# Kernel optimization log

Hardware: AMD Instinct MI355X
Metric: run time of the kernel (lower is better)

## Reference

```python
import jax, jax.numpy as jnp
import numpy as np

C = 4  # n_features_per_level
RES = [128, 256, 512, 1024]  # base_resolution=128, per_level_scale=2, n_levels=4


def grid_sample(grid, pts):
    """Bilinear grid_sample, align_corners=False, zero padding.
    grid: (B, C, H, W); pts: (B, N, 2) with pts[...,0]=x (width), pts[...,1]=y (height).
    Returns (B, C, N)."""
    B, Cc, H, W = grid.shape
    fx = (pts[..., 0] + 1.0) * 0.5 * W - 0.5
    fy = (pts[..., 1] + 1.0) * 0.5 * H - 0.5
    x0 = jnp.floor(fx)
    y0 = jnp.floor(fy)
    wx = (fx - x0)[:, None, :]
    wy = (fy - y0)[:, None, :]
    x0 = x0.astype(jnp.int32)
    y0 = y0.astype(jnp.int32)

    def corner(xi, yi):
        valid = ((xi >= 0) & (xi < W) & (yi >= 0) & (yi < H)).astype(grid.dtype)
        xc = jnp.clip(xi, 0, W - 1)
        yc = jnp.clip(yi, 0, H - 1)
        vals = jax.vmap(lambda g, yy, xx: g[:, yy, xx])(grid, yc, xc)  # (B, C, N)
        return vals * valid[:, None, :]

    v00 = corner(x0, y0)
    v10 = corner(x0 + 1, y0)
    v01 = corner(x0, y0 + 1)
    v11 = corner(x0 + 1, y0 + 1)
    return (v00 * (1 - wx) * (1 - wy) + v10 * wx * (1 - wy)
            + v01 * (1 - wx) * wy + v11 * wx * wy)


def _flat(f):
    # (3, C, N) -> (N, 3*C), matching torch out.reshape(3*C, N).T
    return f.reshape(3 * f.shape[1], f.shape[2]).T


def _forward(x, triplanes, trilines):
    x2 = x * 2.0 - 1.0  # map [0,1] -> [-1,1]
    # plane projections: (xz), (yx), (zy)
    x_pl = jnp.stack([
        jnp.stack([x2[:, 0], x2[:, 2]], -1),
        jnp.stack([x2[:, 1], x2[:, 0]], -1),
        jnp.stack([x2[:, 2], x2[:, 1]], -1)], 0)  # (3, N, 2)
    x_li = jnp.stack([x2[:, 0], x2[:, 1], x2[:, 2]], 0)
    x_li = jnp.stack([x_li, jnp.zeros_like(x_li)], -1)  # (3, N, 2)
    feats = []
    for tp, tl in zip(triplanes, trilines):
        f = _flat(grid_sample(tp, x_pl)) * _flat(grid_sample(tl, x_li))  # (N, 3C)
        feats.append(f)
    return jnp.concatenate(feats, -1)  # (N, 3*C*n_levels)


def setup_inputs() -> dict:
    key = jax.random.key(0)
    ks = jax.random.split(key, 9)
    N = 1 << 20
    d = {"x": jax.random.uniform(ks[0], (N, 3), jnp.float32)}
    for i, r in enumerate(RES):
        d[f"triplane_{i}"] = jax.random.normal(ks[1 + i], (3, C, r, r), jnp.float32)
        d[f"triline_{i}"] = jax.random.normal(ks[5 + i], (3, C, r, 1), jnp.float32)
    return d


def reference(x, triplane_0, triplane_1, triplane_2, triplane_3,
              triline_0, triline_1, triline_2, triline_3):
    triplanes = [triplane_0, triplane_1, triplane_2, triplane_3]
    trilines = [triline_0, triline_1, triline_2, triline_3]
    return _forward(x, triplanes, trilines)
```

## Files before the change

kernel.cpp:

```cpp
#include <hip/hip_runtime.h>
#include <cstdint>


typedef float f32x4 __attribute__((ext_vector_type(4)));

static constexpr int QE0 = 199692;
static constexpr int QE1 = 992280;
static constexpr int QE2 = 4150308;
static constexpr int L3T = 3145728;
static constexpr int TOTAL_SLOTS = QE2 + L3T;
static constexpr int S_OFFF = (QE2 + L3T) * 4;
static constexpr size_t WS1_NEED = (size_t)(S_OFFF + 48) * sizeof(float);

static constexpr int LVL_OFF[4] = {0, 196608, 983040, 4128768};
static constexpr int S_OFF2 = 16711680;
static constexpr size_t WS2_NEED = (size_t)(S_OFF2 + 48) * sizeof(float);
static constexpr int TEXELS = 4177920;

__global__ __launch_bounds__(256) void prep_all(
        const float* __restrict__ tp0, const float* __restrict__ tp1,
        const float* __restrict__ tp2, const float* __restrict__ tp3,
        const float* __restrict__ tl0, const float* __restrict__ tl1,
        const float* __restrict__ tl2, const float* __restrict__ tl3,
        float* __restrict__ ws) {
    int t = blockIdx.x * 256 + threadIdx.x;
    if (t < 48) {
        int ll = t / 12, rem = t % 12, pp = rem >> 2, cc = rem & 3;
        const float* tl = (ll == 0) ? tl0 : (ll == 1) ? tl1 : (ll == 2) ? tl2 : tl3;
        int r = 128 << ll;
        const float* row = tl + (size_t)((pp << 2) + cc) * r;
        int y0 = (r >> 1) - 1;
        ws[S_OFFF + t] = 0.5f * row[y0] + 0.5f * row[y0 + 1];
    }
    if (t >= TOTAL_SLOTS) return;
    float4* ws4 = reinterpret_cast<float4*>(ws);
    if (t < QE2) {
        const float* src; int lvl, base;
        if (t < QE0)      { src = tp0; lvl = 0; base = 0; }
        else if (t < QE1) { src = tp1; lvl = 1; base = QE0; }
        else              { src = tp2; lvl = 2; base = QE1; }
        int lt = t - base;
        int q = lt >> 2, s = lt & 3;
        int r = 128 << lvl, R = r + 1, rr_shift = 2 * (7 + lvl);
        int RR = R * R;
        int p   = q / RR;
        int rem = q - p * RR;
        int yq  = rem / R;
        int xq  = rem - yq * R;
        int tx = xq - 1 + (s & 1);
        int ty = yq - 1 + (s >> 1);
        float4 o = {0.f, 0.f, 0.f, 0.f};
        if ((unsigned)tx < (unsigned)r && (unsigned)ty < (unsigned)r) {
            const float* sp = src + ((size_t)(p << 2) << rr_shift) + (size_t)ty * r + tx;
            o.x = sp[0];
            o.y = sp[(size_t)1 << rr_shift];
            o.z = sp[(size_t)2 << rr_shift];
            o.w = sp[(size_t)3 << rr_shift];
        }
        ws4[t] = o;
    } else {
        int t2 = t - QE2;
        int p  = t2 >> 20;
        int yx = t2 & 0xFFFFF;
        const float* sp = tp3 + ((size_t)(p << 2) << 20) + yx;
        float4 o;
        o.x = sp[0];
        o.y = sp[(size_t)1 << 20];
        o.z = sp[(size_t)2 << 20];
        o.w = sp[(size_t)3 << 20];
        ws4[t] = o;
    }
}

struct BilinW {
    int i00, i10, i01, i11;
    float w00, w10, w01, w11;
};

__device__ __forceinline__ BilinW bilin_weights(int r, float u, float v) {
    float fr = (float)r;
    float fx = (u + 1.0f) * 0.5f * fr - 0.5f;
    float fy = (v + 1.0f) * 0.5f * fr - 0.5f;
    float x0f = floorf(fx), y0f = floorf(fy);
    float wx = fx - x0f, wy = fy - y0f;
    int x0 = (int)x0f, y0 = (int)y0f;
    int x1 = x0 + 1, y1 = y0 + 1;
    float vx0 = ((unsigned)x0 < (unsigned)r) ? 1.0f : 0.0f;
    float vx1 = ((unsigned)x1 < (unsigned)r) ? 1.0f : 0.0f;
    float vy0 = ((unsigned)y0 < (unsigned)r) ? 1.0f : 0.0f;
    float vy1 = ((unsigned)y1 < (unsigned)r) ? 1.0f : 0.0f;
    int x0c = min(max(x0, 0), r - 1), x1c = min(max(x1, 0), r - 1);
    int y0c = min(max(y0, 0), r - 1), y1c = min(max(y1, 0), r - 1);
    BilinW b;
    b.i00 = y0c * r + x0c; b.i10 = y0c * r + x1c;
    b.i01 = y1c * r + x0c; b.i11 = y1c * r + x1c;
    b.w00 = (1.0f - wx) * (1.0f - wy) * vx0 * vy0;
    b.w10 = wx * (1.0f - wy) * vx1 * vy0;
    b.w01 = (1.0f - wx) * wy * vx0 * vy1;
    b.w11 = wx * wy * vx1 * vy1;
    return b;
}

__device__ __forceinline__ float line_w(float t) {
    float fx = (t + 1.0f) * 0.5f - 0.5f;
    float x0f = floorf(fx);
    float wx = fx - x0f;
    int x0 = (int)x0f;
    float w = 0.0f;
    if (x0 == 0) w += 1.0f - wx;
    if (x0 == -1) w += wx;
    return w;
}

template <bool VEC4OUT>
__global__ __launch_bounds__(256) void tri12(const float* __restrict__ x,
                                             const f32x4* __restrict__ ws4,
                                             const float* __restrict__ S,
                                             float* __restrict__ out, int N) {
    int gid = blockIdx.x * 256 + threadIdx.x;
    int n = gid / 12;
    int k = gid - n * 12;
    if (n >= N) return;
    float ax = x[n * 3 + 0] * 2.0f - 1.0f;
    float ay = x[n * 3 + 1] * 2.0f - 1.0f;
    float az = x[n * 3 + 2] * 2.0f - 1.0f;
    int l = k / 3;
    int p = k - l * 3;
    float u = (p == 0) ? ax : (p == 1) ? ay : az;
    float v = (p == 0) ? az : (p == 1) ? ax : ay;
    float lw = line_w(u);
    const f32x4* S4 = reinterpret_cast<const f32x4*>(S);
    f32x4 s = S4[k];

    f32x4 o;
    if (l < 3) {
        int r = 128 << l, R = r + 1;
        float fr = (float)r;
        float fx = (u + 1.0f) * 0.5f * fr - 0.5f;
        float fy = (v + 1.0f) * 0.5f * fr - 0.5f;
        float x0f = floorf(fx), y0f = floorf(fy);
        float wx = fx - x0f, wy = fy - y0f;
        int ix = (int)x0f + 1;
        int iy = (int)y0f + 1;
        ix = min(max(ix, 0), R - 1);
        iy = min(max(iy, 0), R - 1);
        int qbase = (l == 0) ? 0 : (l == 1) ? QE0 : QE1;
        const f32x4* Q = ws4 + qbase + (size_t)((p * R + iy) * R + ix) * 4;
        f32x4 q0 = Q[0], q1 = Q[1], q2 = Q[2], q3 = Q[3];
        float w00 = (1.0f - wx) * (1.0f - wy), w10 = wx * (1.0f - wy);
        float w01 = (1.0f - wx) * wy,          w11 = wx * wy;
        o = q0 * w00 + q1 * w10 + q2 * w01 + q3 * w11;
    } else {
        BilinW b = bilin_weights(1024, u, v);
        const f32x4* G = ws4 + QE2 + (size_t)p * 1048576;
        f32x4 g0 = G[b.i00], g1 = G[b.i10], g2 = G[b.i01], g3 = G[b.i11];
        o = g0 * b.w00 + g1 * b.w10 + g2 * b.w01 + g3 * b.w11;
    }
    o = o * (s * lw);

    if (VEC4OUT) {
        __builtin_nontemporal_store(o, reinterpret_cast<f32x4*>(out) + gid);
    } else {
        size_t base = (size_t)gid * 4;
        out[base + 0] = o.x; out[base + 1] = o.y;
        out[base + 2] = o.z; out[base + 3] = o.w;
    }
}

__global__ __launch_bounds__(256) void repack_all(
        const float* __restrict__ tp0, const float* __restrict__ tp1,
        const float* __restrict__ tp2, const float* __restrict__ tp3,
        const float* __restrict__ tl0, const float* __restrict__ tl1,
        const float* __restrict__ tl2, const float* __restrict__ tl3,
        float* __restrict__ ws) {
    int t = blockIdx.x * 256 + threadIdx.x;
    const float* src; int rr_shift, texoff;
    if (t < 49152)        { src = tp0; rr_shift = 14; texoff = 0; }
    else if (t < 245760)  { src = tp1; rr_shift = 16; texoff = 49152; }
    else if (t < 1032192) { src = tp2; rr_shift = 18; texoff = 245760; }
    else                  { src = tp3; rr_shift = 20; texoff = 1032192; }
    int local = t - texoff;
    int p  = local >> rr_shift;
    int yx = local & ((1 << rr_shift) - 1);
    const float* s0 = src + ((size_t)(p << 2) << rr_shift) + yx;
    float4 o;
    o.x = s0[0];
    o.y = s0[(size_t)1 << rr_shift];
    o.z = s0[(size_t)2 << rr_shift];
    o.w = s0[(size_t)3 << rr_shift];
    reinterpret_cast<float4*>(ws)[t] = o;
    if (t < 48) {
        int ll = t / 12, rem = t % 12, pp = rem >> 2, cc = rem & 3;
        const float* tl = (ll == 0) ? tl0 : (ll == 1) ? tl1 : (ll == 2) ? tl2 : tl3;
        int r = 128 << ll;
        const float* row = tl + (size_t)((pp << 2) + cc) * r;
        int y0 = (r >> 1) - 1;
        ws[S_OFF2 + t] = 0.5f * row[y0] + 0.5f * row[y0 + 1];
    }
}

__device__ __forceinline__ f32x4 bacc(const float4& A, const float4& B2,
                                      const float4& C2, const float4& D,
                                      const BilinW& b, const float4& s, float lwv) {
    f32x4 o;
    o.x = (A.x * b.w00 + B2.x * b.w10 + C2.x * b.w01 + D.x * b.w11) * (s.x * lwv);
    o.y = (A.y * b.w00 + B2.y * b.w10 + C2.y * b.w01 + D.y * b.w11) * (s.y * lwv);
    o.z = (A.z * b.w00 + B2.z * b.w10 + C2.z * b.w01 + D.z * b.w11) * (s.z * lwv);
    o.w = (A.w * b.w00 + B2.w * b.w10 + C2.w * b.w01 + D.w * b.w11) * (s.w * lwv);
    return o;
}

template <bool VEC4OUT>
__global__ __launch_bounds__(256, 2) void tri_split4(
        const float* __restrict__ x, const float4* __restrict__ planes,
        const float* __restrict__ S, float* __restrict__ out, int N) {
    int gid = blockIdx.x * 256 + threadIdx.x;
    int n = gid >> 2;
    int l = gid & 3;
    if (n >= N) return;
    float ax = x[n * 3 + 0] * 2.0f - 1.0f;
    float ay = x[n * 3 + 1] * 2.0f - 1.0f;
    float az = x[n * 3 + 2] * 2.0f - 1.0f;
    const int r = 128 << l;
    const int rr = r * r;
    int texoff = (l == 0) ? 0 : (l == 1) ? 49152 : (l == 2) ? 245760 : 1032192;
    const float4* G0 = planes + texoff;
    const float4* G1 = G0 + rr;
    const float4* G2 = G1 + rr;
    BilinW b0 = bilin_weights(r, ax, az);
    BilinW b1 = bilin_weights(r, ay, ax);
    BilinW b2 = bilin_weights(r, az, ay);
    float4 g0a = G0[b0.i00], g0b = G0[b0.i10], g0c = G0[b0.i01], g0d = G0[b0.i11];
    float4 g1a = G1[b1.i00], g1b = G1[b1.i10], g1c = G1[b1.i01], g1d = G1[b1.i11];
    float4 g2a = G2[b2.i00], g2b = G2[b2.i10], g2c = G2[b2.i01], g2d = G2[b2.i11];
    float lw0 = line_w(ax), lw1 = line_w(ay), lw2 = line_w(az);
    const float4* S4 = reinterpret_cast<const float4*>(S);
    float4 s0 = S4[l * 3 + 0], s1 = S4[l * 3 + 1], s2 = S4[l * 3 + 2];

    f32x4 o0 = bacc(g0a, g0b, g0c, g0d, b0, s0, lw0);
    f32x4 o1 = bacc(g1a, g1b, g1c, g1d, b1, s1, lw1);
    f32x4 o2 = bacc(g2a, g2b, g2c, g2d, b2, s2, lw2);

    size_t base = (size_t)n * 48 + (size_t)l * 12;
    if (VEC4OUT) {
        f32x4* op = reinterpret_cast<f32x4*>(out + base);
        __builtin_nontemporal_store(o0, op);
        __builtin_nontemporal_store(o1, op + 1);
        __builtin_nontemporal_store(o2, op + 2);
    } else {
        out[base + 0] = o0.x; out[base + 1]  = o0.y;
        out[base + 2] = o0.z; out[base + 3]  = o0.w;
        out[base + 4] = o1.x; out[base + 5]  = o1.y;
        out[base + 6] = o1.z; out[base + 7]  = o1.w;
        out[base + 8] = o2.x; out[base + 9]  = o2.y;
        out[base + 10] = o2.z; out[base + 11] = o2.w;
    }
}

__global__ __launch_bounds__(256) void tri_direct(
        const float* __restrict__ x,
        const float* __restrict__ tp0, const float* __restrict__ tp1,
        const float* __restrict__ tp2, const float* __restrict__ tp3,
        const float* __restrict__ tl0, const float* __restrict__ tl1,
        const float* __restrict__ tl2, const float* __restrict__ tl3,
        float* __restrict__ out, int N) {
    int n = blockIdx.x * blockDim.x + threadIdx.x;
    if (n >= N) return;
    float ax = x[n * 3 + 0] * 2.0f - 1.0f;
    float ay = x[n * 3 + 1] * 2.0f - 1.0f;
    float az = x[n * 3 + 2] * 2.0f - 1.0f;
    const float U[3] = {ax, ay, az};
    const float V[3] = {az, ax, ay};
    const float LW[3] = {line_w(ax), line_w(ay), line_w(az)};
    const float* TP[4] = {tp0, tp1, tp2, tp3};
    const float* TL[4] = {tl0, tl1, tl2, tl3};

#pragma unroll
    for (int l = 0; l < 4; ++l) {
        const int r = 128 << l;
        const int rr = r * r;
        const int y0 = (r >> 1) - 1;
#pragma unroll
        for (int p = 0; p < 3; ++p) {
            const float* G = TP[l] + (size_t)(p * 4) * rr;
            BilinW b = bilin_weights(r, U[p], V[p]);
            const float w = LW[p];
#pragma unroll
            for (int c = 0; c < 4; ++c) {
                const float* Gc = G + (size_t)c * rr;
                float acc = Gc[b.i00] * b.w00 + Gc[b.i10] * b.w10 +
                            Gc[b.i01] * b.w01 + Gc[b.i11] * b.w11;
                const float* row = TL[l] + (size_t)((p << 2) + c) * r;
                float s = 0.5f * row[y0] + 0.5f * row[y0 + 1];
                out[(size_t)n * 48 + l * 12 + p * 4 + c] = acc * (s * w);
            }
        }
    }
}

extern "C" void kernel_launch(void* const* d_in, const int* in_sizes, int n_in,
                              void* d_out, int out_size, void* d_ws, size_t ws_size,
                              hipStream_t stream) {
    const float* x = (const float*)d_in[0];
    const float* tp[4];
    const float* tl[4];
    bool interleaved = (n_in >= 9) && (in_sizes[2] == 1536);
    for (int l = 0; l < 4; ++l) {
        if (interleaved) {
            tp[l] = (const float*)d_in[1 + 2 * l];
            tl[l] = (const float*)d_in[2 + 2 * l];
        } else {
            tp[l] = (const float*)d_in[1 + l];
            tl[l] = (const float*)d_in[5 + l];
        }
    }
    int N = in_sizes[0] / 3;
    float* out = (float*)d_out;
    bool out16 = (((uintptr_t)d_out & 15u) == 0);

    if (ws_size >= WS1_NEED && (((uintptr_t)d_ws & 63u) == 0)) {
        float* ws = (float*)d_ws;
        int prep_grid = (TOTAL_SLOTS + 255) / 256;
        prep_all<<<prep_grid, 256, 0, stream>>>(
            tp[0], tp[1], tp[2], tp[3], tl[0], tl[1], tl[2], tl[3], ws);
        long long total = 12LL * N;
        int grid = (int)((total + 255) / 256);
        if (out16) {
            tri12<true><<<grid, 256, 0, stream>>>(
                x, (const f32x4*)ws, ws + S_OFFF, out, N);
        } else {
            tri12<false><<<grid, 256, 0, stream>>>(
                x, (const f32x4*)ws, ws + S_OFFF, out, N);
        }
    } else if (ws_size >= WS2_NEED && (((uintptr_t)d_ws & 15u) == 0)) {
        float* ws = (float*)d_ws;
        repack_all<<<TEXELS / 256, 256, 0, stream>>>(
            tp[0], tp[1], tp[2], tp[3], tl[0], tl[1], tl[2], tl[3], ws);
        long long total = 4LL * N;
        int grid = (int)((total + 255) / 256);
        if (out16) {
            tri_split4<true><<<grid, 256, 0, stream>>>(
                x, (const float4*)ws, ws + S_OFF2, out, N);
        } else {
            tri_split4<false><<<grid, 256, 0, stream>>>(
                x, (const float4*)ws, ws + S_OFF2, out, N);
        }
    } else {
        int grid = (N + 255) / 256;
        tri_direct<<<grid, 256, 0, stream>>>(
            x, tp[0], tp[1], tp[2], tp[3], tl[0], tl[1], tl[2], tl[3], out, N);
    }
}
```

Baseline: 558.3 us.

## Extend corner-quad packed layout to the finest triplane level

Adds a prep kernel that packs all four levels, including the 1024 resolution plane, into corner-quad float4 blocks, plus a gather kernel that reads one contiguous 64-byte quad per sample for every level. This removes the separate four-gather path for level 3 and the divergence between branches. In exchange the workspace grows to roughly 268MB and the prep pass writes about four times the level-3 texel data each call. The old split4 fallback path is removed.

```diff
diff --git a/kernel.cpp b/kernel.cpp
--- a/kernel.cpp
+++ b/kernel.cpp
@@ -3,19 +3,150 @@
 
 
 typedef float f32x4 __attribute__((ext_vector_type(4)));
+
+static constexpr int Q1_0 = 0;
+static constexpr int Q1_1 = 199692;
+static constexpr int Q1_2 = 992280;
+static constexpr int Q1_3 = 4150308;
+static constexpr int Q1_END = 16757808;
+static constexpr int S1_OFF = Q1_END * 4;
+static constexpr size_t WS1_NEED = ((size_t)S1_OFF + 48) * sizeof(float);
 
 static constexpr int QE0 = 199692;
 static constexpr int QE1 = 992280;
 static constexpr int QE2 = 4150308;
 static constexpr int L3T = 3145728;
-static constexpr int TOTAL_SLOTS = QE2 + L3T;
-static constexpr int S_OFFF = (QE2 + L3T) * 4;
-static constexpr size_t WS1_NEED = (size_t)(S_OFFF + 48) * sizeof(float);
-
-static constexpr int LVL_OFF[4] = {0, 196608, 983040, 4128768};
-static constexpr int S_OFF2 = 16711680;
-static constexpr size_t WS2_NEED = (size_t)(S_OFF2 + 48) * sizeof(float);
-static constexpr int TEXELS = 4177920;
+static constexpr int T2_TOTAL = QE2 + L3T;
+static constexpr int S2_OFF = (QE2 + L3T) * 4;
+static constexpr size_t WS2_NEED = (size_t)(S2_OFF + 48) * sizeof(float);
+
+__global__ __launch_bounds__(256) void prep_quads_all(
+        const float* __restrict__ tp0, const float* __restrict__ tp1,
+        const float* __restrict__ tp2, const float* __restrict__ tp3,
+        const float* __restrict__ tl0, const float* __restrict__ tl1,
+        const float* __restrict__ tl2, const float* __restrict__ tl3,
+        float* __restrict__ ws) {
+    int t = blockIdx.x * 256 + threadIdx.x;
+    if (t < 48) {
+        int ll = t / 12, rem = t % 12, pp = rem >> 2, cc = rem & 3;
+        const float* tl = (ll == 0) ? tl0 : (ll == 1) ? tl1 : (ll == 2) ? tl2 : tl3;
+        int r = 128 << ll;
+        const float* row = tl + (size_t)((pp << 2) + cc) * r;
+        int y0 = (r >> 1) - 1;
+        ws[S1_OFF + t] = 0.5f * row[y0] + 0.5f * row[y0 + 1];
+    }
+    if (t >= Q1_END) return;
+    const float* src; int lvl, base;
+    if (t < Q1_1)      { src = tp0; lvl = 0; base = Q1_0; }
+    else if (t < Q1_2) { src = tp1; lvl = 1; base = Q1_1; }
+    else if (t < Q1_3) { src = tp2; lvl = 2; base = Q1_2; }
+    else               { src = tp3; lvl = 3; base = Q1_3; }
+    int lt = t - base;
+    int q = lt >> 2, s = lt & 3;
+    int r = 128 << lvl, R = r + 1, rr_shift = 2 * (7 + lvl);
+    int RR = R * R;
+    int p   = q / RR;
+    int rem = q - p * RR;
+    int yq  = rem / R;
+    int xq  = rem - yq * R;
+    int tx = xq - 1 + (s & 1);
+    int ty = yq - 1 + (s >> 1);
+    float4 o = {0.f, 0.f, 0.f, 0.f};
+    if ((unsigned)tx < (unsigned)r && (unsigned)ty < (unsigned)r) {
+        const float* sp = src + ((size_t)(p << 2) << rr_shift) + (size_t)ty * r + tx;
+        o.x = sp[0];
+        o.y = sp[(size_t)1 << rr_shift];
+        o.z = sp[(size_t)2 << rr_shift];
+        o.w = sp[(size_t)3 << rr_shift];
+    }
+    reinterpret_cast<float4*>(ws)[t] = o;
+}
+
+struct BilinW {
+    int i00, i10, i01, i11;
+    float w00, w10, w01, w11;
+};
+
+__device__ __forceinline__ BilinW bilin_weights(int r, float u, float v) {
+    float fr = (float)r;
+    float fx = (u + 1.0f) * 0.5f * fr - 0.5f;
+    float fy = (v + 1.0f) * 0.5f * fr - 0.5f;
+    float x0f = floorf(fx), y0f = floorf(fy);
+    float wx = fx - x0f, wy = fy - y0f;
+    int x0 = (int)x0f, y0 = (int)y0f;
+    int x1 = x0 + 1, y1 = y0 + 1;
+    float vx0 = ((unsigned)x0 < (unsigned)r) ? 1.0f : 0.0f;
+    float vx1 = ((unsigned)x1 < (unsigned)r) ? 1.0f : 0.0f;
+    float vy0 = ((unsigned)y0 < (unsigned)r) ? 1.0f : 0.0f;
+    float vy1 = ((unsigned)y1 < (unsigned)r) ? 1.0f : 0.0f;
+    int x0c = min(max(x0, 0), r - 1), x1c = min(max(x1, 0), r - 1);
+    int y0c = min(max(y0, 0), r - 1), y1c = min(max(y1, 0), r - 1);
+    BilinW b;
+    b.i00 = y0c * r + x0c; b.i10 = y0c * r + x1c;
+    b.i01 = y1c * r + x0c; b.i11 = y1c * r + x1c;
+    b.w00 = (1.0f - wx) * (1.0f - wy) * vx0 * vy0;
+    b.w10 = wx * (1.0f - wy) * vx1 * vy0;
+    b.w01 = (1.0f - wx) * wy * vx0 * vy1;
+    b.w11 = wx * wy * vx1 * vy1;
+    return b;
+}
+
+__device__ __forceinline__ float line_w(float t) {
+    float fx = (t + 1.0f) * 0.5f - 0.5f;
+    float x0f = floorf(fx);
+    float wx = fx - x0f;
+    int x0 = (int)x0f;
+    float w = 0.0f;
+    if (x0 == 0) w += 1.0f - wx;
+    if (x0 == -1) w += wx;
+    return w;
+}
+
+template <bool VEC4OUT>
+__global__ __launch_bounds__(256) void tri12q(const float* __restrict__ x,
+                                              const f32x4* __restrict__ ws4,
+                                              const float* __restrict__ S,
+                                              float* __restrict__ out, int N) {
+    int gid = blockIdx.x * 256 + threadIdx.x;
+    int n = gid / 12;
+    int k = gid - n * 12;
+    if (n >= N) return;
+    float ax = x[n * 3 + 0] * 2.0f - 1.0f;
+    float ay = x[n * 3 + 1] * 2.0f - 1.0f;
+    float az = x[n * 3 + 2] * 2.0f - 1.0f;
+    int l = k / 3;
+    int p = k - l * 3;
+    float u = (p == 0) ? ax : (p == 1) ? ay : az;
+    float v = (p == 0) ? az : (p == 1) ? ax : ay;
+    float lw = line_w(u);
+    f32x4 s = reinterpret_cast<const f32x4*>(S)[k];
+
+    int r = 128 << l, R = r + 1;
+    float fr = (float)r;
+    float fx = (u + 1.0f) * 0.5f * fr - 0.5f;
+    float fy = (v + 1.0f) * 0.5f * fr - 0.5f;
+    float x0f = floorf(fx), y0f = floorf(fy);
+    float wx = fx - x0f, wy = fy - y0f;
+    int ix = (int)x0f + 1;
+    int iy = (int)y0f + 1;
+    ix = min(max(ix, 0), R - 1);
+    iy = min(max(iy, 0), R - 1);
+    int qbase = (l == 0) ? Q1_0 : (l == 1) ? Q1_1 : (l == 2) ? Q1_2 : Q1_3;
+    const f32x4* Q = ws4 + qbase + (size_t)((p * R + iy) * R + ix) * 4;
+    f32x4 q0 = Q[0], q1 = Q[1], q2 = Q[2], q3 = Q[3];
+    float w00 = (1.0f - wx) * (1.0f - wy), w10 = wx * (1.0f - wy);
+    float w01 = (1.0f - wx) * wy,          w11 = wx * wy;
+    f32x4 o = q0 * w00 + q1 * w10 + q2 * w01 + q3 * w11;
+    o = o * (s * lw);
+
+    if (VEC4OUT) {
+        __builtin_nontemporal_store(o, reinterpret_cast<f32x4*>(out) + gid);
+    } else {
+        size_t base = (size_t)gid * 4;
+        out[base + 0] = o.x; out[base + 1] = o.y;
+        out[base + 2] = o.z; out[base + 3] = o.w;
+    }
+}
 
 __global__ __launch_bounds__(256) void prep_all(
         const float* __restrict__ tp0, const float* __restrict__ tp1,
@@ -30,9 +161,9 @@
         int r = 128 << ll;
         const float* row = tl + (size_t)((pp << 2) + cc) * r;
         int y0 = (r >> 1) - 1;
-        ws[S_OFFF + t] = 0.5f * row[y0] + 0.5f * row[y0 + 1];
-    }
-    if (t >= TOTAL_SLOTS) return;
+        ws[S2_OFF + t] = 0.5f * row[y0] + 0.5f * row[y0 + 1];
+    }
+    if (t >= T2_TOTAL) return;
     float4* ws4 = reinterpret_cast<float4*>(ws);
     if (t < QE2) {
         const float* src; int lvl, base;
@@ -72,46 +203,6 @@
     }
 }
 
-struct BilinW {
-    int i00, i10, i01, i11;
-    float w00, w10, w01, w11;
-};
-
-__device__ __forceinline__ BilinW bilin_weights(int r, float u, float v) {
-    float fr = (float)r;
-    float fx = (u + 1.0f) * 0.5f * fr - 0.5f;
-    float fy = (v + 1.0f) * 0.5f * fr - 0.5f;
-    float x0f = floorf(fx), y0f = floorf(fy);
-    float wx = fx - x0f, wy = fy - y0f;
-    int x0 = (int)x0f, y0 = (int)y0f;
-    int x1 = x0 + 1, y1 = y0 + 1;
-    float vx0 = ((unsigned)x0 < (unsigned)r) ? 1.0f : 0.0f;
-    float vx1 = ((unsigned)x1 < (unsigned)r) ? 1.0f : 0.0f;
-    float vy0 = ((unsigned)y0 < (unsigned)r) ? 1.0f : 0.0f;
-    float vy1 = ((unsigned)y1 < (unsigned)r) ? 1.0f : 0.0f;
-    int x0c = min(max(x0, 0), r - 1), x1c = min(max(x1, 0), r - 1);
-    int y0c = min(max(y0, 0), r - 1), y1c = min(max(y1, 0), r - 1);
-    BilinW b;
-    b.i00 = y0c * r + x0c; b.i10 = y0c * r + x1c;
-    b.i01 = y1c * r + x0c; b.i11 = y1c * r + x1c;
-    b.w00 = (1.0f - wx) * (1.0f - wy) * vx0 * vy0;
-    b.w10 = wx * (1.0f - wy) * vx1 * vy0;
-    b.w01 = (1.0f - wx) * wy * vx0 * vy1;
-    b.w11 = wx * wy * vx1 * vy1;
-    return b;
-}
-
-__device__ __forceinline__ float line_w(float t) {
-    float fx = (t + 1.0f) * 0.5f - 0.5f;
-    float x0f = floorf(fx);
-    float wx = fx - x0f;
-    int x0 = (int)x0f;
-    float w = 0.0f;
-    if (x0 == 0) w += 1.0f - wx;
-    if (x0 == -1) w += wx;
-    return w;
-}
-
 template <bool VEC4OUT>
 __global__ __launch_bounds__(256) void tri12(const float* __restrict__ x,
                                              const f32x4* __restrict__ ws4,
@@ -129,8 +220,7 @@
     float u = (p == 0) ? ax : (p == 1) ? ay : az;
     float v = (p == 0) ? az : (p == 1) ? ax : ay;
     float lw = line_w(u);
-    const f32x4* S4 = reinterpret_cast<const f32x4*>(S);
-    f32x4 s = S4[k];
+    f32x4 s = reinterpret_cast<const f32x4*>(S)[k];
 
     f32x4 o;
     if (l < 3) {
@@ -164,96 +254,6 @@
         size_t base = (size_t)gid * 4;
         out[base + 0] = o.x; out[base + 1] = o.y;
         out[base + 2] = o.z; out[base + 3] = o.w;
-    }
-}
-
-__global__ __launch_bounds__(256) void repack_all(
-        const float* __restrict__ tp0, const float* __restrict__ tp1,
-        const float* __restrict__ tp2, const float* __restrict__ tp3,
-        const float* __restrict__ tl0, const float* __restrict__ tl1,
-        const float* __restrict__ tl2, const float* __restrict__ tl3,
-        float* __restrict__ ws) {
-    int t = blockIdx.x * 256 + threadIdx.x;
-    const float* src; int rr_shift, texoff;
-    if (t < 49152)        { src = tp0; rr_shift = 14; texoff = 0; }
-    else if (t < 245760)  { src = tp1; rr_shift = 16; texoff = 49152; }
-    else if (t < 1032192) { src = tp2; rr_shift = 18; texoff = 245760; }
-    else                  { src = tp3; rr_shift = 20; texoff = 1032192; }
-    int local = t - texoff;
-    int p  = local >> rr_shift;
-    int yx = local & ((1 << rr_shift) - 1);
-    const float* s0 = src + ((size_t)(p << 2) << rr_shift) + yx;
-    float4 o;
-    o.x = s0[0];
-    o.y = s0[(size_t)1 << rr_shift];
-    o.z = s0[(size_t)2 << rr_shift];
-    o.w = s0[(size_t)3 << rr_shift];
-    reinterpret_cast<float4*>(ws)[t] = o;
-    if (t < 48) {
-        int ll = t / 12, rem = t % 12, pp = rem >> 2, cc = rem & 3;
-        const float* tl = (ll == 0) ? tl0 : (ll == 1) ? tl1 : (ll == 2) ? tl2 : tl3;
-        int r = 128 << ll;
-        const float* row = tl + (size_t)((pp << 2) + cc) * r;
-        int y0 = (r >> 1) - 1;
-        ws[S_OFF2 + t] = 0.5f * row[y0] + 0.5f * row[y0 + 1];
-    }
-}
-
-__device__ __forceinline__ f32x4 bacc(const float4& A, const float4& B2,
-                                      const float4& C2, const float4& D,
-                                      const BilinW& b, const float4& s, float lwv) {
-    f32x4 o;
-    o.x = (A.x * b.w00 + B2.x * b.w10 + C2.x * b.w01 + D.x * b.w11) * (s.x * lwv);
-    o.y = (A.y * b.w00 + B2.y * b.w10 + C2.y * b.w01 + D.y * b.w11) * (s.y * lwv);
-    o.z = (A.z * b.w00 + B2.z * b.w10 + C2.z * b.w01 + D.z * b.w11) * (s.z * lwv);
-    o.w = (A.w * b.w00 + B2.w * b.w10 + C2.w * b.w01 + D.w * b.w11) * (s.w * lwv);
-    return o;
-}
-
-template <bool VEC4OUT>
-__global__ __launch_bounds__(256, 2) void tri_split4(
-        const float* __restrict__ x, const float4* __restrict__ planes,
-        const float* __restrict__ S, float* __restrict__ out, int N) {
-    int gid = blockIdx.x * 256 + threadIdx.x;
-    int n = gid >> 2;
-    int l = gid & 3;
-    if (n >= N) return;
-    float ax = x[n * 3 + 0] * 2.0f - 1.0f;
-    float ay = x[n * 3 + 1] * 2.0f - 1.0f;
-    float az = x[n * 3 + 2] * 2.0f - 1.0f;
-    const int r = 128 << l;
-    const int rr = r * r;
-    int texoff = (l == 0) ? 0 : (l == 1) ? 49152 : (l == 2) ? 245760 : 1032192;
-    const float4* G0 = planes + texoff;
-    const float4* G1 = G0 + rr;
-    const float4* G2 = G1 + rr;
-    BilinW b0 = bilin_weights(r, ax, az);
-    BilinW b1 = bilin_weights(r, ay, ax);
-    BilinW b2 = bilin_weights(r, az, ay);
-    float4 g0a = G0[b0.i00], g0b = G0[b0.i10], g0c = G0[b0.i01], g0d = G0[b0.i11];
-    float4 g1a = G1[b1.i00], g1b = G1[b1.i10], g1c = G1[b1.i01], g1d = G1[b1.i11];
-    float4 g2a = G2[b2.i00], g2b = G2[b2.i10], g2c = G2[b2.i01], g2d = G2[b2.i11];
-    float lw0 = line_w(ax), lw1 = line_w(ay), lw2 = line_w(az);
-    const float4* S4 = reinterpret_cast<const float4*>(S);
-    float4 s0 = S4[l * 3 + 0], s1 = S4[l * 3 + 1], s2 = S4[l * 3 + 2];
-
-    f32x4 o0 = bacc(g0a, g0b, g0c, g0d, b0, s0, lw0);
-    f32x4 o1 = bacc(g1a, g1b, g1c, g1d, b1, s1, lw1);
-    f32x4 o2 = bacc(g2a, g2b, g2c, g2d, b2, s2, lw2);
-
-    size_t base = (size_t)n * 48 + (size_t)l * 12;
-    if (VEC4OUT) {
-        f32x4* op = reinterpret_cast<f32x4*>(out + base);
-        __builtin_nontemporal_store(o0, op);
-        __builtin_nontemporal_store(o1, op + 1);
-        __builtin_nontemporal_store(o2, op + 2);
-    } else {
-        out[base + 0] = o0.x; out[base + 1]  = o0.y;
-        out[base + 2] = o0.z; out[base + 3]  = o0.w;
-        out[base + 4] = o1.x; out[base + 5]  = o1.y;
-        out[base + 6] = o1.z; out[base + 7]  = o1.w;
-        out[base + 8] = o2.x; out[base + 9]  = o2.y;
-        out[base + 10] = o2.z; out[base + 11] = o2.w;
     }
 }
 
@@ -320,30 +320,31 @@
 
     if (ws_size >= WS1_NEED && (((uintptr_t)d_ws & 63u) == 0)) {
         float* ws = (float*)d_ws;
-        int prep_grid = (TOTAL_SLOTS + 255) / 256;
+        int prep_grid = (Q1_END + 255) / 256;
+        prep_quads_all<<<prep_grid, 256, 0, stream>>>(
+            tp[0], tp[1], tp[2], tp[3], tl[0], tl[1], tl[2], tl[3], ws);
+        long long total = 12LL * N;
+        int grid = (int)((total + 255) / 256);
+        if (out16) {
+            tri12q<true><<<grid, 256, 0, stream>>>(
+                x, (const f32x4*)ws, ws + S1_OFF, out, N);
+        } else {
+            tri12q<false><<<grid, 256, 0, stream>>>(
+                x, (const f32x4*)ws, ws + S1_OFF, out, N);
+        }
+    } else if (ws_size >= WS2_NEED && (((uintptr_t)d_ws & 63u) == 0)) {
+        float* ws = (float*)d_ws;
+        int prep_grid = (T2_TOTAL + 255) / 256;
         prep_all<<<prep_grid, 256, 0, stream>>>(
             tp[0], tp[1], tp[2], tp[3], tl[0], tl[1], tl[2], tl[3], ws);
         long long total = 12LL * N;
         int grid = (int)((total + 255) / 256);
         if (out16) {
             tri12<true><<<grid, 256, 0, stream>>>(
-                x, (const f32x4*)ws, ws + S_OFFF, out, N);
+                x, (const f32x4*)ws, ws + S2_OFF, out, N);
         } else {
             tri12<false><<<grid, 256, 0, stream>>>(
-                x, (const f32x4*)ws, ws + S_OFFF, out, N);
-        }
-    } else if (ws_size >= WS2_NEED && (((uintptr_t)d_ws & 15u) == 0)) {
-        float* ws = (float*)d_ws;
-        repack_all<<<TEXELS / 256, 256, 0, stream>>>(
-            tp[0], tp[1], tp[2], tp[3], tl[0], tl[1], tl[2], tl[3], ws);
-        long long total = 4LL * N;
-        int grid = (int)((total + 255) / 256);
-        if (out16) {
-            tri_split4<true><<<grid, 256, 0, stream>>>(
-                x, (const float4*)ws, ws + S_OFF2, out, N);
-        } else {
-            tri_split4<false><<<grid, 256, 0, stream>>>(
-                x, (const float4*)ws, ws + S_OFF2, out, N);
+                x, (const f32x4*)ws, ws + S2_OFF, out, N);
         }
     } else {
         int grid = (N + 255) / 256;
```

New measurement: 536.3 us. -3.9%, faster.
